# Performance work log

Measured on AMD Instinct MI355X. Metric: run time of the kernel, lower is better.

The kernel has to match this reference:

```python
import jax, jax.numpy as jnp
import numpy as np

N_ATOMS = 65536
N_BONDS = 131072
N_MOLS = 512
D_IN = 16
D = 128
REPEAT = 3


def _dense(key, fan_in, fan_out):
    kw, kb = jax.random.split(key)
    scale = 1.0 / np.sqrt(fan_in)
    W = jax.random.normal(kw, (fan_in, fan_out), dtype=jnp.float32) * scale
    b = jnp.zeros((fan_out,), dtype=jnp.float32)
    return W, b


def setup_inputs() -> dict:
    key = jax.random.key(0)
    ks = jax.random.split(key, 12)
    atoms = jax.random.normal(ks[0], (N_ATOMS, D_IN), dtype=jnp.float32)
    bond_orders = jax.random.uniform(ks[1], (N_BONDS,), dtype=jnp.float32)
    bond_src = jax.random.randint(ks[2], (N_BONDS,), 0, N_ATOMS, dtype=jnp.int32)
    bond_dst = jax.random.randint(ks[3], (N_BONDS,), 0, N_ATOMS, dtype=jnp.int32)
    atom_mol = jnp.sort(jax.random.randint(ks[4], (N_ATOMS,), 0, N_MOLS, dtype=jnp.int32))
    bond_mol = jnp.sort(jax.random.randint(ks[5], (N_BONDS,), 0, N_MOLS, dtype=jnp.int32))
    W_fe, b_fe = _dense(ks[6], 1, D)      # f_e : bond order -> h_e
    W_fv, b_fv = _dense(ks[7], D_IN, D)   # f_v : atom feats -> h_v
    W_fu, b_fu = _dense(ks[8], D, D)      # f_u : per-mol init from aggregated nodes
    W_e, b_e = _dense(ks[9], 5 * D, D)    # phi_e(h_e, h_e0, h_left, h_right, u)
    W_v, b_v = _dense(ks[10], 4 * D, D)   # phi_v(h_v, h_v0, e_bar_i, u)
    W_u, b_u = _dense(ks[11], 4 * D, D)   # phi_u(h_u, h_u0, e_bar, v_bar)
    return dict(atoms=atoms, bond_orders=bond_orders, W_fe=W_fe, b_fe=b_fe,
                W_fv=W_fv, b_fv=b_fv, W_fu=W_fu, b_fu=b_fu, W_e=W_e, b_e=b_e,
                W_v=W_v, b_v=b_v, W_u=W_u, b_u=b_u,
                bond_src=bond_src, bond_dst=bond_dst,
                atom_mol=atom_mol, bond_mol=bond_mol)


def reference(atoms, bond_orders, W_fe, b_fe, W_fv, b_fv, W_fu, b_fu,
              W_e, b_e, W_v, b_v, W_u, b_u,
              bond_src, bond_dst, atom_mol, bond_mol):
    seg = lambda x, ids, n: jax.ops.segment_sum(x, ids, num_segments=n)
    relu = jax.nn.relu

    # f_e / f_v / f_u initial embeddings
    h_e0 = relu(bond_orders[:, None] @ W_fe + b_fe)           # [E, D]
    h_v0 = relu(atoms @ W_fv + b_fv)                          # [N, D]
    h_u0 = relu(seg(h_v0, atom_mol, N_MOLS) @ W_fu + b_fu)    # [M, D]

    h_e, h_v, h_u = h_e0, h_v0, h_u0
    for _ in range(REPEAT):
        # phi_e(e_k, e_k_0, v_rk, v_sk, u): gather endpoints and per-bond global
        h_left = h_v[bond_src]                                # [E, D]
        h_right = h_v[bond_dst]                               # [E, D]
        u_e = h_u[bond_mol]                                   # [E, D]
        h_e = relu(jnp.concatenate([h_e, h_e0, h_left, h_right, u_e], axis=1) @ W_e + b_e)
        # rho_e_v: sum of updated edges incident to each atom (one-hot mask == scatter-add)
        e_bar_i = seg(h_e, bond_src, N_ATOMS) + seg(h_e, bond_dst, N_ATOMS)  # [N, D]
        # phi_v(v_i, v_i_0, e_bar_i, u)
        h_v = relu(jnp.concatenate([h_v, h_v0, e_bar_i, h_u[atom_mol]], axis=1) @ W_v + b_v)
        # rho_e_u / rho_v_u: per-molecule segment sums
        e_bar = seg(h_e, bond_mol, N_MOLS)                    # [M, D]
        v_bar = seg(h_v, atom_mol, N_MOLS)                    # [M, D]
        # phi_u(u, u_0, e_bar, v_bar)
        h_u = relu(jnp.concatenate([h_u, h_u0, e_bar, v_bar], axis=1) @ W_u + b_u)
    return h_u
```

## Files before the change

kernel.cpp:

```cpp
#include <hip/hip_runtime.h>
#include <hip/hip_bf16.h>
#include <stdint.h>

#define N_ATOMS 65536
#define N_BONDS 131072
#define N_MOLS  512
#define D_IN    16
#define DD      128
#define REPEAT  3
#define PITCH   136

typedef __attribute__((ext_vector_type(8))) short s8b;
typedef __attribute__((ext_vector_type(4))) float f32x4;

__device__ __forceinline__ float us2f(unsigned short s) {
    unsigned int u = ((unsigned int)s) << 16;
    float f; __builtin_memcpy(&f, &u, 4); return f;
}
__device__ __forceinline__ unsigned short f2us(float f) {
    __hip_bfloat16 h = __float2bfloat16(f);
    unsigned short s; __builtin_memcpy(&s, &h, 2); return s;
}
__device__ __forceinline__ void acc8(float* a, uint4 v) {
    unsigned short w[8]; __builtin_memcpy(w, &v, 16);
#pragma unroll
    for (int j = 0; j < 8; j++) a[j] += us2f(w[j]);
}

__device__ __forceinline__ void mfma_store(const unsigned short* xs,
        const unsigned short* __restrict__ Wpk, int wc,
        unsigned short* __restrict__ out, int row0, int tid) {
    int wv = tid >> 6, lane = tid & 63, quad = lane >> 4, l15 = lane & 15;
    f32x4 acc[8][2];
#pragma unroll
    for (int mt = 0; mt < 8; mt++) {
        acc[mt][0] = (f32x4){0.f,0.f,0.f,0.f};
        acc[mt][1] = (f32x4){0.f,0.f,0.f,0.f};
    }
#pragma unroll
    for (int ks = 0; ks < 4; ks++) {
        const unsigned short* wb = Wpk + ((wc * 4 + ks) * 4 + quad) * 1024 + (wv * 32 + l15) * 8;
        s8b b0 = *reinterpret_cast<const s8b*>(wb);
        s8b b1 = *reinterpret_cast<const s8b*>(wb + 128);
#pragma unroll
        for (int mt = 0; mt < 8; mt++) {
            s8b afr = *reinterpret_cast<const s8b*>(&xs[(mt*16 + l15) * PITCH + ks*32 + quad*8]);
            acc[mt][0] = __builtin_amdgcn_mfma_f32_16x16x32_bf16(afr, b0, acc[mt][0], 0, 0, 0);
            acc[mt][1] = __builtin_amdgcn_mfma_f32_16x16x32_bf16(afr, b1, acc[mt][1], 0, 0, 0);
        }
    }
#pragma unroll
    for (int mt = 0; mt < 8; mt++)
#pragma unroll
        for (int r = 0; r < 4; r++) {
            int row = row0 + mt*16 + quad*4 + r;
#pragma unroll
            for (int nt = 0; nt < 2; nt++) {
                int col = wv*32 + nt*16 + l15;
                out[(size_t)row * DD + col] = f2us(acc[mt][nt][r]);
            }
        }
}


__device__ __forceinline__ void pack_one(const float* W, unsigned short* Wpk, int idx) {
    int k = idx >> 7, n = idx & 127;
    int c = k >> 7, ks = (k >> 5) & 3, quad = (k >> 3) & 3, j = k & 7;
    Wpk[(((c * 4 + ks) * 4 + quad) * 128 + n) * 8 + j] = f2us(W[k * 128 + n]);
}
__global__ void k_pack2(const float* __restrict__ We, const float* __restrict__ Wv,
                        unsigned short* __restrict__ WeP, unsigned short* __restrict__ WvP) {
    int idx = blockIdx.x * 256 + threadIdx.x;
    const int NE = 640 * 128;
    if (idx < NE) pack_one(We, WeP, idx);
    else if (idx < NE + 512 * 128) pack_one(Wv, WvP, idx - NE);
}

__global__ void k_deg(const int* __restrict__ bsrc, const int* __restrict__ bdst,
                      int* __restrict__ deg) {
    int e = blockIdx.x * 256 + threadIdx.x;
    atomicAdd(&deg[bsrc[e]], 1);
    atomicAdd(&deg[bdst[e]], 1);
}

__global__ void k_scan1(const int* __restrict__ deg, int* __restrict__ bsum) {
    __shared__ int red[256];
    int t = threadIdx.x;
    red[t] = deg[blockIdx.x * 256 + t];
    __syncthreads();
    for (int s = 128; s > 0; s >>= 1) {
        if (t < s) red[t] += red[t + s];
        __syncthreads();
    }
    if (t == 0) bsum[blockIdx.x] = red[0];
}

__global__ void k_scan3b(const int* __restrict__ deg, const int* __restrict__ bsum,
                         int* __restrict__ rowptr, int* __restrict__ cursor) {
    __shared__ int sb[256];
    __shared__ int s[256];
    int t = threadIdx.x;
    sb[t] = bsum[t];
    __syncthreads();
    for (int off = 1; off < 256; off <<= 1) {
        int v = (t >= off) ? sb[t - off] : 0;
        __syncthreads();
        sb[t] += v;
        __syncthreads();
    }
    int boff = sb[blockIdx.x] - bsum[blockIdx.x];
    int i = blockIdx.x * 256 + t;
    int d = deg[i];
    s[t] = d;
    __syncthreads();
    for (int off = 1; off < 256; off <<= 1) {
        int v = (t >= off) ? s[t - off] : 0;
        __syncthreads();
        s[t] += v;
        __syncthreads();
    }
    int val = boff + s[t] - d;
    rowptr[i] = val;
    cursor[i] = val;
    if (i == N_ATOMS - 1) rowptr[N_ATOMS] = val + d;
}

__global__ void k_fill(const int* __restrict__ bsrc, const int* __restrict__ bdst,
                       int* __restrict__ cursor, int* __restrict__ adj) {
    int e = blockIdx.x * 256 + threadIdx.x;
    int p = atomicAdd(&cursor[bsrc[e]], 1); adj[p] = e;
    int q = atomicAdd(&cursor[bdst[e]], 1); adj[q] = e;
}

__global__ void k_molptr2(const int* __restrict__ bmol, const int* __restrict__ amol,
                          int* __restrict__ bptr, int* __restrict__ aptr) {
    int m = threadIdx.x;
    if (m > N_MOLS) return;
    const int* ids = blockIdx.x ? amol : bmol;
    int rows = blockIdx.x ? N_ATOMS : N_BONDS;
    int* out = blockIdx.x ? aptr : bptr;
    int lo = 0, hi = rows;
    while (lo < hi) {
        int mid = (lo + hi) >> 1;
        if (ids[mid] < m) lo = mid + 1; else hi = mid;
    }
    out[m] = lo;
}


__global__ void k_init_he(const float* __restrict__ bo, const float* __restrict__ Wfe,
                          const float* __restrict__ bfe, unsigned short* __restrict__ he) {
    int idx = blockIdx.x * 256 + threadIdx.x;
    int e = idx >> 7, d = idx & 127;
    he[idx] = f2us(fmaxf(fmaf(bo[e], Wfe[d], bfe[d]), 0.f));
}

__global__ __launch_bounds__(256) void k_nodes_f(
        const float* __restrict__ atoms, const float* __restrict__ Wfv,
        const float* __restrict__ bfv,
        const unsigned short* __restrict__ WvP, const unsigned short* __restrict__ WeP,
        unsigned short* __restrict__ hv, unsigned short* __restrict__ yv0,
        unsigned short* __restrict__ Zs, unsigned short* __restrict__ Zd,
        float* __restrict__ node_sum) {
    __shared__ __align__(16) unsigned short xs[128 * PITCH];
    int tid = threadIdx.x;
    int gid = blockIdx.x * 256 + tid;
    if (gid < N_MOLS * DD) node_sum[gid] = 0.f;
    int n0 = blockIdx.x * 128;
    for (int t = 0; t < 8; t++) {
        int u = tid + t * 256;
        int i = u >> 4, g = (u & 15) * 8;
        int row = n0 + i;
        float a[D_IN];
#pragma unroll
        for (int k = 0; k < D_IN; k++) a[k] = atoms[(size_t)row * D_IN + k];
        unsigned short tmp[8];
#pragma unroll
        for (int j = 0; j < 8; j++) {
            float acc1 = bfv[g + j];
#pragma unroll
            for (int k = 0; k < D_IN; k++)
                acc1 = fmaf(a[k], Wfv[k*DD + g + j], acc1);
            tmp[j] = f2us(fmaxf(acc1, 0.f));
        }
        uint4 val; __builtin_memcpy(&val, tmp, 16);
        *reinterpret_cast<uint4*>(&xs[i * PITCH + g]) = val;
        *reinterpret_cast<uint4*>(hv + (size_t)row * DD + g) = val;
    }
    __syncthreads();
    mfma_store(xs, WvP, 1, yv0, n0, tid);
    mfma_store(xs, WeP, 2, Zs, n0, tid);
    mfma_store(xs, WeP, 3, Zd, n0, tid);
}

__global__ __launch_bounds__(256) void k_molsum_s(const unsigned short* __restrict__ x,
                                                  const int* __restrict__ mptr,
                                                  float* __restrict__ out, int S) {
    __shared__ float red[16 * 128];
    int m = blockIdx.x / S, s = blockIdx.x - m * S;
    int b = mptr[m], e = mptr[m + 1];
    int len = (e - b + S - 1) / S;
    int r0 = b + s * len;
    int r1 = min(r0 + len, e);
    int rl = threadIdx.x >> 4, g = threadIdx.x & 15;
    float acc[8] = {0,0,0,0,0,0,0,0};
    for (int r = r0 + rl; r < r1; r += 16)
        acc8(acc, *reinterpret_cast<const uint4*>(x + (size_t)r * DD + g * 8));
#pragma unroll
    for (int j = 0; j < 8; j++) red[rl * 128 + g * 8 + j] = acc[j];
    __syncthreads();
    if (threadIdx.x < 128) {
        int col = threadIdx.x;
        float sum = 0.f;
#pragma unroll
        for (int i = 0; i < 16; i++) sum += red[i * 128 + col];
        atomicAdd(&out[(size_t)m * DD + col], sum);
    }
}

__global__ __launch_bounds__(256) void k_mol_init_f(
        const float* __restrict__ ns, const float* __restrict__ Wfu,
        const float* __restrict__ bfu,
        const float* __restrict__ We, const float* __restrict__ be,
        const float* __restrict__ Wv, const float* __restrict__ bv,
        float* __restrict__ hu0, float* __restrict__ yue, float* __restrict__ yuv,
        float* __restrict__ ebar, float* __restrict__ vbar) {
    __shared__ float hrow[2 * DD];
    int tid = threadIdx.x;
    int ml = tid >> 7, d = tid & 127;
    int m = blockIdx.x * 2 + ml;
    ebar[m*DD + d] = 0.f;
    vbar[m*DD + d] = 0.f;
    float acc = bfu[d];
    for (int k = 0; k < DD; k++)
        acc = fmaf(ns[m*DD + k], Wfu[k*DD + d], acc);
    float v = fmaxf(acc, 0.f);
    hu0[m*DD + d] = v;
    hrow[ml*DD + d] = v;
    __syncthreads();
    float ae = be[d], av = bv[d];
    for (int k = 0; k < DD; k++) {
        float h = hrow[ml*DD + k];
        ae = fmaf(h, We[(512 + k)*DD + d], ae);
        av = fmaf(h, Wv[(384 + k)*DD + d], av);
    }
    yue[m*DD + d] = ae;
    yuv[m*DD + d] = av;
}

__global__ __launch_bounds__(256) void k_phi_e(
        unsigned short* __restrict__ he,
        const float* __restrict__ bo, const float* __restrict__ Wfe,
        const float* __restrict__ bfe,
        const unsigned short* __restrict__ Zs, const unsigned short* __restrict__ Zd,
        const unsigned short* __restrict__ Wpk, const float* __restrict__ yue,
        const int* __restrict__ bsrc, const int* __restrict__ bdst,
        const int* __restrict__ bmol, float* __restrict__ ebar) {
    __shared__ __align__(16) unsigned short xs[128 * PITCH];
    __shared__ int ssrc[128], sdst[128], smol[128];
    __shared__ float sbo[128];
    int tid = threadIdx.x;
    int e0 = blockIdx.x * 128;
    if (tid < 128) {
        ssrc[tid] = bsrc[e0 + tid];
        sdst[tid] = bdst[e0 + tid];
        smol[tid] = bmol[e0 + tid];
        sbo[tid]  = bo[e0 + tid];
    }
    int wv = tid >> 6, lane = tid & 63, quad = lane >> 4, l15 = lane & 15;
    f32x4 acc[8][2];
#pragma unroll
    for (int mt = 0; mt < 8; mt++) {
        acc[mt][0] = (f32x4){0.f,0.f,0.f,0.f};
        acc[mt][1] = (f32x4){0.f,0.f,0.f,0.f};
    }
    for (int t = 0; t < 8; t++) {
        int u = tid + t * 256;
        int i = u >> 4, g = (u & 15) * 8;
        *reinterpret_cast<uint4*>(&xs[i * PITCH + g]) =
            *reinterpret_cast<const uint4*>(he + (size_t)(e0 + i) * DD + g);
    }
    __syncthreads();
#pragma unroll
    for (int ks = 0; ks < 4; ks++) {
        const unsigned short* wb = Wpk + ((0 * 4 + ks) * 4 + quad) * 1024 + (wv * 32 + l15) * 8;
        s8b b0 = *reinterpret_cast<const s8b*>(wb);
        s8b b1 = *reinterpret_cast<const s8b*>(wb + 128);
#pragma unroll
        for (int mt = 0; mt < 8; mt++) {
            s8b afr = *reinterpret_cast<const s8b*>(&xs[(mt*16 + l15) * PITCH + ks*32 + quad*8]);
            acc[mt][0] = __builtin_amdgcn_mfma_f32_16x16x32_bf16(afr, b0, acc[mt][0], 0, 0, 0);
            acc[mt][1] = __builtin_amdgcn_mfma_f32_16x16x32_bf16(afr, b1, acc[mt][1], 0, 0, 0);
        }
    }
    __syncthreads();
    for (int t = 0; t < 8; t++) {
        int u = tid + t * 256;
        int i = u >> 4, g = (u & 15) * 8;
        float b = sbo[i];
        unsigned short tmp[8];
#pragma unroll
        for (int j = 0; j < 8; j++)
            tmp[j] = f2us(fmaxf(fmaf(b, Wfe[g + j], bfe[g + j]), 0.f));
        uint4 val; __builtin_memcpy(&val, tmp, 16);
        *reinterpret_cast<uint4*>(&xs[i * PITCH + g]) = val;
    }
    __syncthreads();
#pragma unroll
    for (int ks = 0; ks < 4; ks++) {
        const unsigned short* wb = Wpk + ((1 * 4 + ks) * 4 + quad) * 1024 + (wv * 32 + l15) * 8;
        s8b b0 = *reinterpret_cast<const s8b*>(wb);
        s8b b1 = *reinterpret_cast<const s8b*>(wb + 128);
#pragma unroll
        for (int mt = 0; mt < 8; mt++) {
            s8b afr = *reinterpret_cast<const s8b*>(&xs[(mt*16 + l15) * PITCH + ks*32 + quad*8]);
            acc[mt][0] = __builtin_amdgcn_mfma_f32_16x16x32_bf16(afr, b0, acc[mt][0], 0, 0, 0);
            acc[mt][1] = __builtin_amdgcn_mfma_f32_16x16x32_bf16(afr, b1, acc[mt][1], 0, 0, 0);
        }
    }
    __syncthreads();
    for (int t = 0; t < 8; t++) {
        int u = tid + t * 256;
        int i = u >> 4, g = (u & 15) * 8;
        float s[8] = {0,0,0,0,0,0,0,0};
        acc8(s, *reinterpret_cast<const uint4*>(Zs + (size_t)ssrc[i] * DD + g));
        acc8(s, *reinterpret_cast<const uint4*>(Zd + (size_t)sdst[i] * DD + g));
        const float* yr = yue + (size_t)smol[i] * DD + g;
        float4 y0 = *reinterpret_cast<const float4*>(yr);
        float4 y1 = *reinterpret_cast<const float4*>(yr + 4);
        s[0] += y0.x; s[1] += y0.y; s[2] += y0.z; s[3] += y0.w;
        s[4] += y1.x; s[5] += y1.y; s[6] += y1.z; s[7] += y1.w;
        unsigned short tmp[8];
#pragma unroll
        for (int j = 0; j < 8; j++) tmp[j] = f2us(s[j]);
        uint4 val; __builtin_memcpy(&val, tmp, 16);
        *reinterpret_cast<uint4*>(&xs[i * PITCH + g]) = val;
    }
    __syncthreads();
#pragma unroll
    for (int nt = 0; nt < 2; nt++) {
        int col = wv*32 + nt*16 + l15;
        float run = 0.f;
        int cur = smol[quad * 4];
#pragma unroll
        for (int mt = 0; mt < 8; mt++)
#pragma unroll
            for (int r = 0; r < 4; r++) {
                int rl = mt*16 + quad*4 + r;
                float v = fmaxf(acc[mt][nt][r] + us2f(xs[rl * PITCH + col]), 0.f);
                he[(size_t)(e0 + rl) * DD + col] = f2us(v);
                int m = smol[rl];
                if (m != cur) { atomicAdd(&ebar[(size_t)cur * DD + col], run); run = 0.f; cur = m; }
                run += v;
            }
        atomicAdd(&ebar[(size_t)cur * DD + col], run);
    }
}

__global__ __launch_bounds__(256) void k_ebar(const unsigned short* __restrict__ he,
                                              const int* __restrict__ rowptr,
                                              const int* __restrict__ adj,
                                              unsigned short* __restrict__ ebar_i) {
    int n = blockIdx.x * 16 + (threadIdx.x >> 4);
    int g = threadIdx.x & 15;
    int b = rowptr[n], e = rowptr[n + 1];
    float acc[8] = {0,0,0,0,0,0,0,0};
    int j = b;
    for (; j + 3 < e; j += 4) {
        uint4 v0 = *reinterpret_cast<const uint4*>(he + (size_t)adj[j]     * DD + g * 8);
        uint4 v1 = *reinterpret_cast<const uint4*>(he + (size_t)adj[j + 1] * DD + g * 8);
        uint4 v2 = *reinterpret_cast<const uint4*>(he + (size_t)adj[j + 2] * DD + g * 8);
        uint4 v3 = *reinterpret_cast<const uint4*>(he + (size_t)adj[j + 3] * DD + g * 8);
        acc8(acc, v0); acc8(acc, v1); acc8(acc, v2); acc8(acc, v3);
    }
    for (; j < e; j++)
        acc8(acc, *reinterpret_cast<const uint4*>(he + (size_t)adj[j] * DD + g * 8));
    unsigned short o[8];
#pragma unroll
    for (int k = 0; k < 8; k++) o[k] = f2us(acc[k]);
    uint4 ov; __builtin_memcpy(&ov, o, 16);
    *reinterpret_cast<uint4*>(ebar_i + (size_t)n * DD + g * 8) = ov;
}

__global__ __launch_bounds__(256) void k_phi_v(
        unsigned short* __restrict__ hv, const unsigned short* __restrict__ ebar_i,
        const unsigned short* __restrict__ yv0,
        const unsigned short* __restrict__ WvP, const unsigned short* __restrict__ WeP,
        const float* __restrict__ yuv, const int* __restrict__ amol,
        float* __restrict__ vbar,
        unsigned short* __restrict__ Zs, unsigned short* __restrict__ Zd, int do_z) {
    __shared__ __align__(16) unsigned short xs[128 * PITCH];
    __shared__ int smol[128];
    int tid = threadIdx.x;
    int n0 = blockIdx.x * 128;
    if (tid < 128) smol[tid] = amol[n0 + tid];
    int wv = tid >> 6, lane = tid & 63, quad = lane >> 4, l15 = lane & 15;
    f32x4 acc[8][2];
#pragma unroll
    for (int mt = 0; mt < 8; mt++) {
        acc[mt][0] = (f32x4){0.f,0.f,0.f,0.f};
        acc[mt][1] = (f32x4){0.f,0.f,0.f,0.f};
    }
    const unsigned short* bases[2] = { hv + (size_t)n0 * DD, ebar_i + (size_t)n0 * DD };
    const int wcs[2] = {0, 2};
    for (int c = 0; c < 2; c++) {
        if (c) __syncthreads();
        for (int t = 0; t < 8; t++) {
            int u = tid + t * 256;
            int i = u >> 4, g = (u & 15) * 8;
            *reinterpret_cast<uint4*>(&xs[i * PITCH + g]) =
                *reinterpret_cast<const uint4*>(bases[c] + (size_t)i * DD + g);
        }
        __syncthreads();
        int WC = wcs[c];
#pragma unroll
        for (int ks = 0; ks < 4; ks++) {
            const unsigned short* wb = WvP + ((WC * 4 + ks) * 4 + quad) * 1024 + (wv * 32 + l15) * 8;
            s8b b0 = *reinterpret_cast<const s8b*>(wb);
            s8b b1 = *reinterpret_cast<const s8b*>(wb + 128);
#pragma unroll
            for (int mt = 0; mt < 8; mt++) {
                s8b afr = *reinterpret_cast<const s8b*>(&xs[(mt*16 + l15) * PITCH + ks*32 + quad*8]);
                acc[mt][0] = __builtin_amdgcn_mfma_f32_16x16x32_bf16(afr, b0, acc[mt][0], 0, 0, 0);
                acc[mt][1] = __builtin_amdgcn_mfma_f32_16x16x32_bf16(afr, b1, acc[mt][1], 0, 0, 0);
            }
        }
    }
    __syncthreads();
    for (int t = 0; t < 8; t++) {
        int u = tid + t * 256;
        int i = u >> 4, g = (u & 15) * 8;
        float s[8] = {0,0,0,0,0,0,0,0};
        acc8(s, *reinterpret_cast<const uint4*>(yv0 + (size_t)(n0 + i) * DD + g));
        const float* yr = yuv + (size_t)smol[i] * DD + g;
        float4 y0 = *reinterpret_cast<const float4*>(yr);
        float4 y1 = *reinterpret_cast<const float4*>(yr + 4);
        s[0] += y0.x; s[1] += y0.y; s[2] += y0.z; s[3] += y0.w;
        s[4] += y1.x; s[5] += y1.y; s[6] += y1.z; s[7] += y1.w;
        unsigned short tmp[8];
#pragma unroll
        for (int j = 0; j < 8; j++) tmp[j] = f2us(s[j]);
        uint4 val; __builtin_memcpy(&val, tmp, 16);
        *reinterpret_cast<uint4*>(&xs[i * PITCH + g]) = val;
    }
    __syncthreads();
#pragma unroll
    for (int nt = 0; nt < 2; nt++) {
        int col = wv*32 + nt*16 + l15;
        float run = 0.f;
        int cur = smol[quad * 4];
#pragma unroll
        for (int mt = 0; mt < 8; mt++)
#pragma unroll
            for (int r = 0; r < 4; r++) {
                int rl = mt*16 + quad*4 + r;
                float v = fmaxf(acc[mt][nt][r] + us2f(xs[rl * PITCH + col]), 0.f);
                unsigned short vb = f2us(v);
                hv[(size_t)(n0 + rl) * DD + col] = vb;
                xs[rl * PITCH + col] = vb;
                int m = smol[rl];
                if (m != cur) { atomicAdd(&vbar[(size_t)cur * DD + col], run); run = 0.f; cur = m; }
                run += v;
            }
        atomicAdd(&vbar[(size_t)cur * DD + col], run);
    }
    if (do_z) {
        __syncthreads();
        mfma_store(xs, WeP, 2, Zs, n0, tid);
        mfma_store(xs, WeP, 3, Zd, n0, tid);
    }
}

__global__ __launch_bounds__(256) void k_phi_u_f(
        const float* __restrict__ hu_in, const float* __restrict__ hu0,
        float* __restrict__ ebar, float* __restrict__ vbar,
        const float* __restrict__ Wu, const float* __restrict__ bu,
        const float* __restrict__ We, const float* __restrict__ be,
        const float* __restrict__ Wv, const float* __restrict__ bv,
        float* __restrict__ hu_out, float* __restrict__ dout,
        float* __restrict__ yue, float* __restrict__ yuv) {
    __shared__ float hrow[2 * DD];
    int tid = threadIdx.x;
    int ml = tid >> 7, d = tid & 127;
    int m = blockIdx.x * 2 + ml;
    float acc = bu[d];
    const float* segs[4] = { hu_in + m*DD, hu0 + m*DD, ebar + m*DD, vbar + m*DD };
    for (int s = 0; s < 4; s++) {
        const float* x = segs[s];
        const float* W = Wu + (s*DD)*DD + d;
        for (int k = 0; k < DD; k++)
            acc = fmaf(x[k], W[k*DD], acc);
    }
    float v = fmaxf(acc, 0.f);
    hu_out[m*DD + d] = v;
    dout[m*DD + d] = v;
    hrow[ml*DD + d] = v;
    __syncthreads();
    ebar[m*DD + d] = 0.f;
    vbar[m*DD + d] = 0.f;
    float ae = be[d], av = bv[d];
    for (int k = 0; k < DD; k++) {
        float h = hrow[ml*DD + k];
        ae = fmaf(h, We[(512 + k)*DD + d], ae);
        av = fmaf(h, Wv[(384 + k)*DD + d], av);
    }
    yue[m*DD + d] = ae;
    yuv[m*DD + d] = av;
}


extern "C" void kernel_launch(void* const* d_in, const int* in_sizes, int n_in,
                              void* d_out, int out_size, void* d_ws, size_t ws_size,
                              hipStream_t stream) {
    const float* atoms = (const float*)d_in[0];
    const float* bo    = (const float*)d_in[1];
    const float* Wfe   = (const float*)d_in[2];
    const float* bfe   = (const float*)d_in[3];
    const float* Wfv   = (const float*)d_in[4];
    const float* bfv   = (const float*)d_in[5];
    const float* Wfu   = (const float*)d_in[6];
    const float* bfu   = (const float*)d_in[7];
    const float* We    = (const float*)d_in[8];
    const float* be    = (const float*)d_in[9];
    const float* Wv    = (const float*)d_in[10];
    const float* bv    = (const float*)d_in[11];
    const float* Wu    = (const float*)d_in[12];
    const float* bu    = (const float*)d_in[13];
    const int* bsrc    = (const int*)d_in[14];
    const int* bdst    = (const int*)d_in[15];
    const int* amol    = (const int*)d_in[16];
    const int* bmol    = (const int*)d_in[17];

    char* p = (char*)d_ws;
    auto alloc = [&](size_t bytes) {
        char* r = p;
        p += (bytes + 255) & ~(size_t)255;
        return r;
    };
    unsigned short* he     = (unsigned short*)alloc((size_t)N_BONDS * DD * 2);
    unsigned short* hv     = (unsigned short*)alloc((size_t)N_ATOMS * DD * 2);
    unsigned short* yv0    = (unsigned short*)alloc((size_t)N_ATOMS * DD * 2);
    unsigned short* Zs     = (unsigned short*)alloc((size_t)N_ATOMS * DD * 2);
    unsigned short* Zd     = (unsigned short*)alloc((size_t)N_ATOMS * DD * 2);
    unsigned short* ebar_i = (unsigned short*)alloc((size_t)N_ATOMS * DD * 2);
    unsigned short* WeP    = (unsigned short*)alloc((size_t)640 * DD * 2);
    unsigned short* WvP    = (unsigned short*)alloc((size_t)512 * DD * 2);
    int* deg      = (int*)alloc((size_t)N_ATOMS * 4);
    int* rowptr   = (int*)alloc((size_t)(N_ATOMS + 1) * 4);
    int* cursor   = (int*)alloc((size_t)N_ATOMS * 4);
    int* adj      = (int*)alloc((size_t)2 * N_BONDS * 4);
    int* bmol_ptr = (int*)alloc((size_t)(N_MOLS + 1) * 4);
    int* amol_ptr = (int*)alloc((size_t)(N_MOLS + 1) * 4);
    int* bsum     = (int*)alloc((size_t)256 * 4);
    float* node_sum = (float*)alloc((size_t)N_MOLS * DD * 4);
    float* hu0   = (float*)alloc((size_t)N_MOLS * DD * 4);
    float* huA   = (float*)alloc((size_t)N_MOLS * DD * 4);
    float* huB   = (float*)alloc((size_t)N_MOLS * DD * 4);
    float* ebar  = (float*)alloc((size_t)N_MOLS * DD * 4);
    float* vbar  = (float*)alloc((size_t)N_MOLS * DD * 4);
    float* yue   = (float*)alloc((size_t)N_MOLS * DD * 4);
    float* yuv   = (float*)alloc((size_t)N_MOLS * DD * 4);

    hipMemsetAsync(deg, 0, (size_t)N_ATOMS * 4, stream);
    k_deg<<<N_BONDS/256, 256, 0, stream>>>(bsrc, bdst, deg);
    k_scan1<<<256, 256, 0, stream>>>(deg, bsum);
    k_scan3b<<<256, 256, 0, stream>>>(deg, bsum, rowptr, cursor);
    k_fill<<<N_BONDS/256, 256, 0, stream>>>(bsrc, bdst, cursor, adj);
    k_molptr2<<<2, 1024, 0, stream>>>(bmol, amol, bmol_ptr, amol_ptr);

    k_pack2<<<(640*DD + 512*DD)/256, 256, 0, stream>>>(We, Wv, WeP, WvP);

    k_init_he<<<(N_BONDS*DD)/256, 256, 0, stream>>>(bo, Wfe, bfe, he);
    k_nodes_f<<<N_ATOMS/128, 256, 0, stream>>>(atoms, Wfv, bfv, WvP, WeP,
                                               hv, yv0, Zs, Zd, node_sum);
    k_molsum_s<<<N_MOLS*2, 256, 0, stream>>>(hv, amol_ptr, node_sum, 2);
    k_mol_init_f<<<N_MOLS/2, 256, 0, stream>>>(node_sum, Wfu, bfu, We, be, Wv, bv,
                                               hu0, yue, yuv, ebar, vbar);

    const float* hu_in = hu0; float* hu_out = huA;

    for (int r = 0; r < REPEAT; r++) {
        k_phi_e<<<N_BONDS/128, 256, 0, stream>>>(he, bo, Wfe, bfe, Zs, Zd, WeP, yue,
                                                 bsrc, bdst, bmol, ebar);
        k_ebar<<<N_ATOMS/16, 256, 0, stream>>>(he, rowptr, adj, ebar_i);
        k_phi_v<<<N_ATOMS/128, 256, 0, stream>>>(hv, ebar_i, yv0, WvP, WeP, yuv,
                                                 amol, vbar, Zs, Zd, (r < REPEAT - 1) ? 1 : 0);
        k_phi_u_f<<<N_MOLS/2, 256, 0, stream>>>(hu_in, hu0, ebar, vbar, Wu, bu,
                                                We, be, Wv, bv,
                                                hu_out, (float*)d_out, yue, yuv);
        hu_in = hu_out; hu_out = (hu_out == huA) ? huB : huA;
    }
}
```

Measured before the change: 498.6 us.

## Replace CSR build with fixed-width adjacency and fuse initial edge embedding

Replaces the degree/scan/fill CSR construction with a single atomic fill into a fixed 32-slot adjacency list per atom, zeroing degrees inside the weight-pack kernel. Removes the separate initial edge-embedding kernel by having the first phi_e iteration compute he0 in shared memory and use it for both edge inputs. This cuts several setup launches and a full edge-feature write and read. It risks dropping edges for any atom with degree above 32 and spreads adjacency reads over a strided layout.

```diff
diff --git a/kernel.cpp b/kernel.cpp
--- a/kernel.cpp
+++ b/kernel.cpp
@@ -9,6 +9,7 @@
 #define DD      128
 #define REPEAT  3
 #define PITCH   136
+#define ADJW    32
 
 typedef __attribute__((ext_vector_type(8))) short s8b;
 typedef __attribute__((ext_vector_type(4))) float f32x4;
@@ -69,67 +70,23 @@
     Wpk[(((c * 4 + ks) * 4 + quad) * 128 + n) * 8 + j] = f2us(W[k * 128 + n]);
 }
 __global__ void k_pack2(const float* __restrict__ We, const float* __restrict__ Wv,
-                        unsigned short* __restrict__ WeP, unsigned short* __restrict__ WvP) {
+                        unsigned short* __restrict__ WeP, unsigned short* __restrict__ WvP,
+                        int* __restrict__ deg) {
     int idx = blockIdx.x * 256 + threadIdx.x;
+    if (idx < N_ATOMS) deg[idx] = 0;
     const int NE = 640 * 128;
     if (idx < NE) pack_one(We, WeP, idx);
     else if (idx < NE + 512 * 128) pack_one(Wv, WvP, idx - NE);
 }
 
-__global__ void k_deg(const int* __restrict__ bsrc, const int* __restrict__ bdst,
-                      int* __restrict__ deg) {
+__global__ void k_fill_fw(const int* __restrict__ bsrc, const int* __restrict__ bdst,
+                          int* __restrict__ deg, int* __restrict__ adj) {
     int e = blockIdx.x * 256 + threadIdx.x;
-    atomicAdd(&deg[bsrc[e]], 1);
-    atomicAdd(&deg[bdst[e]], 1);
-}
-
-__global__ void k_scan1(const int* __restrict__ deg, int* __restrict__ bsum) {
-    __shared__ int red[256];
-    int t = threadIdx.x;
-    red[t] = deg[blockIdx.x * 256 + t];
-    __syncthreads();
-    for (int s = 128; s > 0; s >>= 1) {
-        if (t < s) red[t] += red[t + s];
-        __syncthreads();
-    }
-    if (t == 0) bsum[blockIdx.x] = red[0];
-}
-
-__global__ void k_scan3b(const int* __restrict__ deg, const int* __restrict__ bsum,
-                         int* __restrict__ rowptr, int* __restrict__ cursor) {
-    __shared__ int sb[256];
-    __shared__ int s[256];
-    int t = threadIdx.x;
-    sb[t] = bsum[t];
-    __syncthreads();
-    for (int off = 1; off < 256; off <<= 1) {
-        int v = (t >= off) ? sb[t - off] : 0;
-        __syncthreads();
-        sb[t] += v;
-        __syncthreads();
-    }
-    int boff = sb[blockIdx.x] - bsum[blockIdx.x];
-    int i = blockIdx.x * 256 + t;
-    int d = deg[i];
-    s[t] = d;
-    __syncthreads();
-    for (int off = 1; off < 256; off <<= 1) {
-        int v = (t >= off) ? s[t - off] : 0;
-        __syncthreads();
-        s[t] += v;
-        __syncthreads();
-    }
-    int val = boff + s[t] - d;
-    rowptr[i] = val;
-    cursor[i] = val;
-    if (i == N_ATOMS - 1) rowptr[N_ATOMS] = val + d;
-}
-
-__global__ void k_fill(const int* __restrict__ bsrc, const int* __restrict__ bdst,
-                       int* __restrict__ cursor, int* __restrict__ adj) {
-    int e = blockIdx.x * 256 + threadIdx.x;
-    int p = atomicAdd(&cursor[bsrc[e]], 1); adj[p] = e;
-    int q = atomicAdd(&cursor[bdst[e]], 1); adj[q] = e;
+    int s = bsrc[e], d = bdst[e];
+    int p = atomicAdd(&deg[s], 1);
+    if (p < ADJW) adj[(size_t)s * ADJW + p] = e;
+    int q = atomicAdd(&deg[d], 1);
+    if (q < ADJW) adj[(size_t)d * ADJW + q] = e;
 }
 
 __global__ void k_molptr2(const int* __restrict__ bmol, const int* __restrict__ amol,
@@ -147,13 +104,6 @@
     out[m] = lo;
 }
 
-
-__global__ void k_init_he(const float* __restrict__ bo, const float* __restrict__ Wfe,
-                          const float* __restrict__ bfe, unsigned short* __restrict__ he) {
-    int idx = blockIdx.x * 256 + threadIdx.x;
-    int e = idx >> 7, d = idx & 127;
-    he[idx] = f2us(fmaxf(fmaf(bo[e], Wfe[d], bfe[d]), 0.f));
-}
 
 __global__ __launch_bounds__(256) void k_nodes_f(
         const float* __restrict__ atoms, const float* __restrict__ Wfv,
@@ -255,7 +205,7 @@
         const unsigned short* __restrict__ Zs, const unsigned short* __restrict__ Zd,
         const unsigned short* __restrict__ Wpk, const float* __restrict__ yue,
         const int* __restrict__ bsrc, const int* __restrict__ bdst,
-        const int* __restrict__ bmol, float* __restrict__ ebar) {
+        const int* __restrict__ bmol, float* __restrict__ ebar, int r0) {
     __shared__ __align__(16) unsigned short xs[128 * PITCH];
     __shared__ int ssrc[128], sdst[128], smol[128];
     __shared__ float sbo[128];
@@ -274,49 +224,54 @@
         acc[mt][0] = (f32x4){0.f,0.f,0.f,0.f};
         acc[mt][1] = (f32x4){0.f,0.f,0.f,0.f};
     }
-    for (int t = 0; t < 8; t++) {
-        int u = tid + t * 256;
-        int i = u >> 4, g = (u & 15) * 8;
-        *reinterpret_cast<uint4*>(&xs[i * PITCH + g]) =
-            *reinterpret_cast<const uint4*>(he + (size_t)(e0 + i) * DD + g);
-    }
-    __syncthreads();
-#pragma unroll
-    for (int ks = 0; ks < 4; ks++) {
-        const unsigned short* wb = Wpk + ((0 * 4 + ks) * 4 + quad) * 1024 + (wv * 32 + l15) * 8;
-        s8b b0 = *reinterpret_cast<const s8b*>(wb);
-        s8b b1 = *reinterpret_cast<const s8b*>(wb + 128);
-#pragma unroll
-        for (int mt = 0; mt < 8; mt++) {
-            s8b afr = *reinterpret_cast<const s8b*>(&xs[(mt*16 + l15) * PITCH + ks*32 + quad*8]);
-            acc[mt][0] = __builtin_amdgcn_mfma_f32_16x16x32_bf16(afr, b0, acc[mt][0], 0, 0, 0);
-            acc[mt][1] = __builtin_amdgcn_mfma_f32_16x16x32_bf16(afr, b1, acc[mt][1], 0, 0, 0);
-        }
-    }
-    __syncthreads();
-    for (int t = 0; t < 8; t++) {
-        int u = tid + t * 256;
-        int i = u >> 4, g = (u & 15) * 8;
-        float b = sbo[i];
-        unsigned short tmp[8];
-#pragma unroll
-        for (int j = 0; j < 8; j++)
-            tmp[j] = f2us(fmaxf(fmaf(b, Wfe[g + j], bfe[g + j]), 0.f));
-        uint4 val; __builtin_memcpy(&val, tmp, 16);
-        *reinterpret_cast<uint4*>(&xs[i * PITCH + g]) = val;
-    }
-    __syncthreads();
-#pragma unroll
-    for (int ks = 0; ks < 4; ks++) {
-        const unsigned short* wb = Wpk + ((1 * 4 + ks) * 4 + quad) * 1024 + (wv * 32 + l15) * 8;
-        s8b b0 = *reinterpret_cast<const s8b*>(wb);
-        s8b b1 = *reinterpret_cast<const s8b*>(wb + 128);
-#pragma unroll
-        for (int mt = 0; mt < 8; mt++) {
-            s8b afr = *reinterpret_cast<const s8b*>(&xs[(mt*16 + l15) * PITCH + ks*32 + quad*8]);
-            acc[mt][0] = __builtin_amdgcn_mfma_f32_16x16x32_bf16(afr, b0, acc[mt][0], 0, 0, 0);
-            acc[mt][1] = __builtin_amdgcn_mfma_f32_16x16x32_bf16(afr, b1, acc[mt][1], 0, 0, 0);
-        }
+
+    auto mfma_chunk = [&](int WC) {
+#pragma unroll
+        for (int ks = 0; ks < 4; ks++) {
+            const unsigned short* wb = Wpk + ((WC * 4 + ks) * 4 + quad) * 1024 + (wv * 32 + l15) * 8;
+            s8b b0 = *reinterpret_cast<const s8b*>(wb);
+            s8b b1 = *reinterpret_cast<const s8b*>(wb + 128);
+#pragma unroll
+            for (int mt = 0; mt < 8; mt++) {
+                s8b afr = *reinterpret_cast<const s8b*>(&xs[(mt*16 + l15) * PITCH + ks*32 + quad*8]);
+                acc[mt][0] = __builtin_amdgcn_mfma_f32_16x16x32_bf16(afr, b0, acc[mt][0], 0, 0, 0);
+                acc[mt][1] = __builtin_amdgcn_mfma_f32_16x16x32_bf16(afr, b1, acc[mt][1], 0, 0, 0);
+            }
+        }
+    };
+    auto stage_he0 = [&]() {
+        for (int t = 0; t < 8; t++) {
+            int u = tid + t * 256;
+            int i = u >> 4, g = (u & 15) * 8;
+            float b = sbo[i];
+            unsigned short tmp[8];
+#pragma unroll
+            for (int j = 0; j < 8; j++)
+                tmp[j] = f2us(fmaxf(fmaf(b, Wfe[g + j], bfe[g + j]), 0.f));
+            uint4 val; __builtin_memcpy(&val, tmp, 16);
+            *reinterpret_cast<uint4*>(&xs[i * PITCH + g]) = val;
+        }
+    };
+
+    if (r0) {
+        __syncthreads();
+        stage_he0();
+        __syncthreads();
+        mfma_chunk(0);
+        mfma_chunk(1);
+    } else {
+        for (int t = 0; t < 8; t++) {
+            int u = tid + t * 256;
+            int i = u >> 4, g = (u & 15) * 8;
+            *reinterpret_cast<uint4*>(&xs[i * PITCH + g]) =
+                *reinterpret_cast<const uint4*>(he + (size_t)(e0 + i) * DD + g);
+        }
+        __syncthreads();
+        mfma_chunk(0);
+        __syncthreads();
+        stage_he0();
+        __syncthreads();
+        mfma_chunk(1);
     }
     __syncthreads();
     for (int t = 0; t < 8; t++) {
@@ -358,23 +313,24 @@
 }
 
 __global__ __launch_bounds__(256) void k_ebar(const unsigned short* __restrict__ he,
-                                              const int* __restrict__ rowptr,
+                                              const int* __restrict__ deg,
                                               const int* __restrict__ adj,
                                               unsigned short* __restrict__ ebar_i) {
     int n = blockIdx.x * 16 + (threadIdx.x >> 4);
     int g = threadIdx.x & 15;
-    int b = rowptr[n], e = rowptr[n + 1];
+    int dn = min(deg[n], ADJW);
+    const int* ap = adj + (size_t)n * ADJW;
     float acc[8] = {0,0,0,0,0,0,0,0};
-    int j = b;
-    for (; j + 3 < e; j += 4) {
-        uint4 v0 = *reinterpret_cast<const uint4*>(he + (size_t)adj[j]     * DD + g * 8);
-        uint4 v1 = *reinterpret_cast<const uint4*>(he + (size_t)adj[j + 1] * DD + g * 8);
-        uint4 v2 = *reinterpret_cast<const uint4*>(he + (size_t)adj[j + 2] * DD + g * 8);
-        uint4 v3 = *reinterpret_cast<const uint4*>(he + (size_t)adj[j + 3] * DD + g * 8);
+    int j = 0;
+    for (; j + 3 < dn; j += 4) {
+        uint4 v0 = *reinterpret_cast<const uint4*>(he + (size_t)ap[j]     * DD + g * 8);
+        uint4 v1 = *reinterpret_cast<const uint4*>(he + (size_t)ap[j + 1] * DD + g * 8);
+        uint4 v2 = *reinterpret_cast<const uint4*>(he + (size_t)ap[j + 2] * DD + g * 8);
+        uint4 v3 = *reinterpret_cast<const uint4*>(he + (size_t)ap[j + 3] * DD + g * 8);
         acc8(acc, v0); acc8(acc, v1); acc8(acc, v2); acc8(acc, v3);
     }
-    for (; j < e; j++)
-        acc8(acc, *reinterpret_cast<const uint4*>(he + (size_t)adj[j] * DD + g * 8));
+    for (; j < dn; j++)
+        acc8(acc, *reinterpret_cast<const uint4*>(he + (size_t)ap[j] * DD + g * 8));
     unsigned short o[8];
 #pragma unroll
     for (int k = 0; k < 8; k++) o[k] = f2us(acc[k]);
@@ -546,12 +502,9 @@
     unsigned short* WeP    = (unsigned short*)alloc((size_t)640 * DD * 2);
     unsigned short* WvP    = (unsigned short*)alloc((size_t)512 * DD * 2);
     int* deg      = (int*)alloc((size_t)N_ATOMS * 4);
-    int* rowptr   = (int*)alloc((size_t)(N_ATOMS + 1) * 4);
-    int* cursor   = (int*)alloc((size_t)N_ATOMS * 4);
-    int* adj      = (int*)alloc((size_t)2 * N_BONDS * 4);
+    int* adj      = (int*)alloc((size_t)N_ATOMS * ADJW * 4);
     int* bmol_ptr = (int*)alloc((size_t)(N_MOLS + 1) * 4);
     int* amol_ptr = (int*)alloc((size_t)(N_MOLS + 1) * 4);
-    int* bsum     = (int*)alloc((size_t)256 * 4);
     float* node_sum = (float*)alloc((size_t)N_MOLS * DD * 4);
     float* hu0   = (float*)alloc((size_t)N_MOLS * DD * 4);
     float* huA   = (float*)alloc((size_t)N_MOLS * DD * 4);
@@ -561,16 +514,10 @@
     float* yue   = (float*)alloc((size_t)N_MOLS * DD * 4);
     float* yuv   = (float*)alloc((size_t)N_MOLS * DD * 4);
 
-    hipMemsetAsync(deg, 0, (size_t)N_ATOMS * 4, stream);
-    k_deg<<<N_BONDS/256, 256, 0, stream>>>(bsrc, bdst, deg);
-    k_scan1<<<256, 256, 0, stream>>>(deg, bsum);
-    k_scan3b<<<256, 256, 0, stream>>>(deg, bsum, rowptr, cursor);
-    k_fill<<<N_BONDS/256, 256, 0, stream>>>(bsrc, bdst, cursor, adj);
+    k_pack2<<<(640*DD + 512*DD)/256, 256, 0, stream>>>(We, Wv, WeP, WvP, deg);
+    k_fill_fw<<<N_BONDS/256, 256, 0, stream>>>(bsrc, bdst, deg, adj);
     k_molptr2<<<2, 1024, 0, stream>>>(bmol, amol, bmol_ptr, amol_ptr);
 
-    k_pack2<<<(640*DD + 512*DD)/256, 256, 0, stream>>>(We, Wv, WeP, WvP);
-
-    k_init_he<<<(N_BONDS*DD)/256, 256, 0, stream>>>(bo, Wfe, bfe, he);
     k_nodes_f<<<N_ATOMS/128, 256, 0, stream>>>(atoms, Wfv, bfv, WvP, WeP,
                                                hv, yv0, Zs, Zd, node_sum);
     k_molsum_s<<<N_MOLS*2, 256, 0, stream>>>(hv, amol_ptr, node_sum, 2);
@@ -581,8 +528,8 @@
 
     for (int r = 0; r < REPEAT; r++) {
         k_phi_e<<<N_BONDS/128, 256, 0, stream>>>(he, bo, Wfe, bfe, Zs, Zd, WeP, yue,
-                                                 bsrc, bdst, bmol, ebar);
-        k_ebar<<<N_ATOMS/16, 256, 0, stream>>>(he, rowptr, adj, ebar_i);
+                                                 bsrc, bdst, bmol, ebar, (r == 0) ? 1 : 0);
+        k_ebar<<<N_ATOMS/16, 256, 0, stream>>>(he, deg, adj, ebar_i);
         k_phi_v<<<N_ATOMS/128, 256, 0, stream>>>(hv, ebar_i, yv0, WvP, WeP, yuv,
                                                  amol, vbar, Zs, Zd, (r < REPEAT - 1) ? 1 : 0);
         k_phi_u_f<<<N_MOLS/2, 256, 0, stream>>>(hu_in, hu0, ebar, vbar, Wu, bu,
```

Measured after the change: 505.8 us. Within noise of the previous version (+1.4%).
